# Kernel optimization log

Measured on AMD Instinct MI355X. Metric: run time of the kernel, lower is better.

Reference implementation:

```python
import jax, jax.numpy as jnp
import numpy as np

EMBED_DIM = 1024
N_HEADS = 16
HEAD_DIM = EMBED_DIM // N_HEADS
SCALE = 1.0 / np.sqrt(HEAD_DIM)


def setup_inputs() -> dict:
    key = jax.random.key(0)
    ks = jax.random.split(key, 11)
    B, S, D = 4, 2048, EMBED_DIM
    lim = 1.0 / np.sqrt(D)
    def lin(kk):
        kw, kb = jax.random.split(kk)
        W = jax.random.uniform(kw, (D, D), jnp.float32, -lim, lim)
        b = jax.random.uniform(kb, (D,), jnp.float32, -lim, lim)
        return W, b
    Wq, bq = lin(ks[0])
    Wk, bk = lin(ks[1])
    Wv, bv = lin(ks[2])
    Wo, bo = lin(ks[3])
    q = jax.random.normal(ks[4], (B, S, D), jnp.float32)
    k = jax.random.normal(ks[5], (B, S, D), jnp.float32)
    v = jax.random.normal(ks[6], (B, S, D), jnp.float32)
    return {"q": q, "k": k, "v": v,
            "Wq": Wq, "bq": bq, "Wk": Wk, "bk": bk,
            "Wv": Wv, "bv": bv, "Wo": Wo, "bo": bo}


def reference(q, k, v, Wq, bq, Wk, bk, Wv, bv, Wo, bo):
    B, Sq, D = q.shape
    Sk = k.shape[1]
    # linear projections (torch Linear: x @ W.T + b)
    qh = (q @ Wq.T + bq).reshape(B, Sq, N_HEADS, HEAD_DIM).transpose(0, 2, 1, 3)
    kh = (k @ Wk.T + bk).reshape(B, Sk, N_HEADS, HEAD_DIM).transpose(0, 2, 1, 3)
    vh = (v @ Wv.T + bv).reshape(B, Sk, N_HEADS, HEAD_DIM).transpose(0, 2, 1, 3)
    # scaled dot-product attention, no mask, dropout_p=0
    scores = jnp.einsum('bhqd,bhkd->bhqk', qh, kh) * SCALE  # [B,H,Sq,Sk]
    weights = jax.nn.softmax(scores, axis=-1)
    ctx = jnp.einsum('bhqk,bhkd->bhqd', weights, vh)
    ctx = ctx.transpose(0, 2, 1, 3).reshape(B, Sq, D)
    return ctx @ Wo.T + bo
```

## Files before the change

### kernel.cpp

```cpp
#include <hip/hip_runtime.h>
#include <hip/hip_bf16.h>
#include <stdint.h>

#define B_SZ 4
#define SEQ  2048
#define DM   1024
#define NH   16
#define HD   64
#define MTOT (B_SZ*SEQ)
#define QS_LOG2E 0.18033688011112042f
#define M0SHIFT  24.0f

typedef __attribute__((ext_vector_type(8))) short bf16x8;
typedef __attribute__((ext_vector_type(4))) float f32x4;

#if __has_builtin(__builtin_amdgcn_exp2f)
__device__ __forceinline__ float fexp2(float x) { return __builtin_amdgcn_exp2f(x); }
#else
__device__ __forceinline__ float fexp2(float x) {
  float r; asm("v_exp_f32 %0, %1" : "=v"(r) : "v"(x)); return r;
}
#endif

__device__ __forceinline__ unsigned short f2b(float f) {
  union { float f; unsigned int i; } v; v.f = f;
  unsigned int r = v.i + 0x7fffu + ((v.i >> 16) & 1u);
  return (unsigned short)(r >> 16);
}

#define GPTR __attribute__((address_space(1)))
#define LPTR __attribute__((address_space(3)))
__device__ __forceinline__ void gl_lds16(const void* g, void* l) {
  __builtin_amdgcn_global_load_lds((GPTR const unsigned int*)g,
                                   (LPTR unsigned int*)l, 16, 0, 0);
}

__device__ __forceinline__ void conv_body(const float* __restrict__ in,
                                          unsigned short* __restrict__ out, int n) {
  int i = (blockIdx.x * 256 + threadIdx.x) * 8;
  int stride = gridDim.x * 256 * 8;
  for (; i < n; i += stride) {
    float4 x = *(const float4*)(in + i);
    float4 y = *(const float4*)(in + i + 4);
    ushort4 u0; u0.x = f2b(x.x); u0.y = f2b(x.y); u0.z = f2b(x.z); u0.w = f2b(x.w);
    ushort4 u1; u1.x = f2b(y.x); u1.y = f2b(y.y); u1.z = f2b(y.z); u1.w = f2b(y.w);
    *(ushort4*)(out + i)     = u0;
    *(ushort4*)(out + i + 4) = u1;
  }
}
__global__ __launch_bounds__(256) void conv7(
    const float* __restrict__ q, const float* __restrict__ k, const float* __restrict__ v,
    const float* __restrict__ Wq, const float* __restrict__ Wk,
    const float* __restrict__ Wv, const float* __restrict__ Wo,
    unsigned short* __restrict__ oq, unsigned short* __restrict__ ok,
    unsigned short* __restrict__ ov, unsigned short* __restrict__ oWq,
    unsigned short* __restrict__ oWk, unsigned short* __restrict__ oWv,
    unsigned short* __restrict__ oWo, int nAct, int nW) {
  const int z = blockIdx.z;
  const float* in = (z == 0) ? q : (z == 1) ? k : (z == 2) ? v
                  : (z == 3) ? Wq : (z == 4) ? Wk : (z == 5) ? Wv : Wo;
  unsigned short* out = (z == 0) ? oq : (z == 1) ? ok : (z == 2) ? ov
                      : (z == 3) ? oWq : (z == 4) ? oWk : (z == 5) ? oWv : oWo;
  conv_body(in, out, (z < 3) ? nAct : nW);
}
__global__ __launch_bounds__(256) void conv4(const float* __restrict__ a,
                                             const float* __restrict__ b,
                                             const float* __restrict__ c,
                                             const float* __restrict__ d,
                                             unsigned short* __restrict__ oa,
                                             unsigned short* __restrict__ ob,
                                             unsigned short* __restrict__ oc,
                                             unsigned short* __restrict__ od,
                                             int n) {
  const float* in = (blockIdx.z == 0) ? a : (blockIdx.z == 1) ? b
                  : (blockIdx.z == 2) ? c : d;
  unsigned short* out = (blockIdx.z == 0) ? oa : (blockIdx.z == 1) ? ob
                      : (blockIdx.z == 2) ? oc : od;
  conv_body(in, out, n);
}

__device__ __forceinline__ void stage_glds(const unsigned short* __restrict__ src,
                                           int ld, char* lds, int t) {
  const int gbase = t & ~63;
  const int lane  = t & 63;
  #pragma unroll
  for (int i = 0; i < 4; ++i) {
    int gb  = i*256 + gbase;
    int g   = gb + lane;
    int row = g >> 3;
    int cg  = (g & 7) ^ (row & 7);
    gl_lds16(src + (size_t)row*ld + cg*8, lds + (size_t)gb*16);
  }
}
__device__ __forceinline__ void stage_f32(const float* __restrict__ src, int ld,
                                          unsigned short* lds, int t) {
  #pragma unroll
  for (int i = 0; i < 8; ++i) {
    int e   = i*1024 + t*4;
    int row = e >> 6;
    int c4  = (e >> 2) & 15;
    float4 f = *(const float4*)(src + (size_t)row*ld + c4*4);
    ushort4 u;
    u.x = f2b(f.x); u.y = f2b(f.y); u.z = f2b(f.z); u.w = f2b(f.w);
    int hi = (row*64 + c4*4) ^ ((row & 7) << 3);
    *(ushort4*)&lds[hi] = u;
  }
}

__device__ __forceinline__ void gemm_core_bb(
    const unsigned short* __restrict__ X, const unsigned short* __restrict__ W,
    const float* __restrict__ bias, unsigned short* __restrict__ C,
    float oscale, int m0, int n0, int t,
    unsigned short* As, unsigned short* Bs)
{
  const int lane = t & 63;
  const int w    = t >> 6;
  const int wm   = w >> 1, wn = w & 1;

  f32x4 acc[4][4] = {};

  for (int k0 = 0; k0 < DM; k0 += 64) {
    __syncthreads();
    stage_glds(X + (size_t)m0*DM + k0, DM, (char*)As, t);
    stage_glds(W + (size_t)n0*DM + k0, DM, (char*)Bs, t);
    __syncthreads();

    #pragma unroll
    for (int kk = 0; kk < 2; ++kk) {
      bf16x8 af[4], bfr[4];
      #pragma unroll
      for (int mt = 0; mt < 4; ++mt) {
        int r  = wm*64 + mt*16 + (lane & 15);
        int hi = (r*64 + kk*32 + (lane >> 4)*8) ^ ((r & 7) << 3);
        af[mt] = *(const bf16x8*)&As[hi];
      }
      #pragma unroll
      for (int nt = 0; nt < 4; ++nt) {
        int r  = wn*64 + nt*16 + (lane & 15);
        int hi = (r*64 + kk*32 + (lane >> 4)*8) ^ ((r & 7) << 3);
        bfr[nt] = *(const bf16x8*)&Bs[hi];
      }
      #pragma unroll
      for (int mt = 0; mt < 4; ++mt)
        #pragma unroll
        for (int nt = 0; nt < 4; ++nt)
          acc[mt][nt] = __builtin_amdgcn_mfma_f32_16x16x32_bf16(
              af[mt], bfr[nt], acc[mt][nt], 0, 0, 0);
    }
  }

  #pragma unroll
  for (int nt = 0; nt < 4; ++nt) {
    int col = n0 + wn*64 + nt*16 + (lane & 15);
    float bv = bias[col];
    #pragma unroll
    for (int mt = 0; mt < 4; ++mt) {
      #pragma unroll
      for (int j = 0; j < 4; ++j) {
        int rrow = m0 + wm*64 + mt*16 + (lane >> 4)*4 + j;
        C[(size_t)rrow*DM + col] = f2b((acc[mt][nt][j] + bv) * oscale);
      }
    }
  }
}

__global__ __launch_bounds__(256, 2) void gemm_qkv(
    const unsigned short* __restrict__ Xb, const unsigned short* __restrict__ Wb,
    const float* __restrict__ b0, const float* __restrict__ b1,
    const float* __restrict__ b2, unsigned short* __restrict__ Cb, float os0)
{
  __shared__ __align__(16) unsigned short As[128*64];
  __shared__ __align__(16) unsigned short Bs[128*64];
  const int z = blockIdx.z;
  const size_t MD  = (size_t)MTOT * DM;
  const size_t WSZ = (size_t)DM * DM;
  const unsigned short* X = Xb + (size_t)z * MD;
  const unsigned short* W = Wb + (size_t)z * WSZ;
  const float* bias = (z == 0) ? b0 : (z == 1) ? b1 : b2;
  unsigned short* C = Cb + (size_t)z * MD;
  float oscale = (z == 0) ? os0 : 1.0f;
  gemm_core_bb(X, W, bias, C, oscale,
               blockIdx.y * 128, blockIdx.x * 128, threadIdx.x, As, Bs);
}

template<int AF32, int BF32, int OUTF32>
__global__ __launch_bounds__(256, 2) void gemm_bias(
    const void* __restrict__ Xv,
    const void* __restrict__ Wv,
    const float* __restrict__ bias,
    void* __restrict__ Cout,
    int M, int N, int Kd, float oscale)
{
  __shared__ __align__(16) unsigned short As[128*64];
  __shared__ __align__(16) unsigned short Bs[128*64];
  const int t    = threadIdx.x;
  const int lane = t & 63;
  const int w    = t >> 6;
  const int wm   = w >> 1, wn = w & 1;
  const int m0   = blockIdx.y * 128;
  const int n0   = blockIdx.x * 128;

  f32x4 acc[4][4] = {};

  for (int k0 = 0; k0 < Kd; k0 += 64) {
    __syncthreads();
    if (AF32) stage_f32((const float*)Xv + (size_t)m0*Kd + k0, Kd, As, t);
    else      stage_glds((const unsigned short*)Xv + (size_t)m0*Kd + k0, Kd, (char*)As, t);
    if (BF32) stage_f32((const float*)Wv + (size_t)n0*Kd + k0, Kd, Bs, t);
    else      stage_glds((const unsigned short*)Wv + (size_t)n0*Kd + k0, Kd, (char*)Bs, t);
    __syncthreads();

    #pragma unroll
    for (int kk = 0; kk < 2; ++kk) {
      bf16x8 af[4], bfr[4];
      #pragma unroll
      for (int mt = 0; mt < 4; ++mt) {
        int r  = wm*64 + mt*16 + (lane & 15);
        int hi = (r*64 + kk*32 + (lane >> 4)*8) ^ ((r & 7) << 3);
        af[mt] = *(const bf16x8*)&As[hi];
      }
      #pragma unroll
      for (int nt = 0; nt < 4; ++nt) {
        int r  = wn*64 + nt*16 + (lane & 15);
        int hi = (r*64 + kk*32 + (lane >> 4)*8) ^ ((r & 7) << 3);
        bfr[nt] = *(const bf16x8*)&Bs[hi];
      }
      #pragma unroll
      for (int mt = 0; mt < 4; ++mt)
        #pragma unroll
        for (int nt = 0; nt < 4; ++nt)
          acc[mt][nt] = __builtin_amdgcn_mfma_f32_16x16x32_bf16(
              af[mt], bfr[nt], acc[mt][nt], 0, 0, 0);
    }
  }

  #pragma unroll
  for (int nt = 0; nt < 4; ++nt) {
    int col = n0 + wn*64 + nt*16 + (lane & 15);
    float bv = bias[col];
    #pragma unroll
    for (int mt = 0; mt < 4; ++mt) {
      #pragma unroll
      for (int j = 0; j < 4; ++j) {
        int rrow = m0 + wm*64 + mt*16 + (lane >> 4)*4 + j;
        float val = (acc[mt][nt][j] + bv) * oscale;
        if (OUTF32)
          ((float*)Cout)[(size_t)rrow*N + col] = val;
        else
          ((unsigned short*)Cout)[(size_t)rrow*N + col] = f2b(val);
      }
    }
  }
}

__global__ __launch_bounds__(256, 2) void attn_fwd(
    const unsigned short* __restrict__ Qb,
    const unsigned short* __restrict__ Kb,
    const unsigned short* __restrict__ Vb,
    unsigned short* __restrict__ Ob)
{
  __shared__ __align__(16) unsigned short Buf[4][64*64];

  const int t    = threadIdx.x;
  const int lane = t & 63;
  const int w    = t >> 6;
  const int l15  = lane & 15;
  const int quad = lane >> 4;

  const int id   = blockIdx.x + (int)gridDim.x * blockIdx.y;
  const int r_   = id & 7;
  const int j_   = id >> 3;
  const int bh   = r_*8 + (j_ >> 4);
  const int qt   = j_ & 15;
  const int b    = bh >> 4, h = bh & 15;
  const int q0   = qt * 128;
  const int gbase = t & ~63;

  const size_t headoff = ((size_t)b*SEQ)*DM + (size_t)h*HD;
  const unsigned short* Qh = Qb + headoff;
  const unsigned short* Kh = Kb + headoff;
  const unsigned short* Vh = Vb + headoff;

  const int jp   = (t & 31) * 2;
  const int seg  = t >> 5;
  const int slot0 = ((jp >> 5) & 1)*32 + ((jp >> 2) & 3)*8 + ((jp >> 4) & 1)*4 + (jp & 3);
  const unsigned short* vsrc = Vh + (size_t)jp*DM + seg*8;

  {
    unsigned short* Qlds = &Buf[2][0];
    #pragma unroll
    for (int i = 0; i < 4; ++i) {
      int gb  = i*256 + gbase;
      int g   = gb + lane;
      int row = g >> 3;
      int cg  = (g & 7) ^ (row & 7);
      gl_lds16(Qh + (size_t)(q0 + row)*DM + cg*8, (char*)Qlds + (size_t)gb*16);
    }
  }
  bf16x8 pvA0 = *(const bf16x8*)(vsrc);
  bf16x8 pvA1 = *(const bf16x8*)(vsrc + DM);
  bf16x8 pvB0 = *(const bf16x8*)(vsrc + 64*DM);
  bf16x8 pvB1 = *(const bf16x8*)(vsrc + 65*DM);
  __syncthreads();

  bf16x8 qfA[2], qfB[2];
  {
    const unsigned short* Qlds = &Buf[2][0];
    #pragma unroll
    for (int kk = 0; kk < 2; ++kk) {
      int rA  = w*32 + l15;
      int rB  = w*32 + 16 + l15;
      qfA[kk] = *(const bf16x8*)&Qlds[(rA*64 + kk*32 + quad*8) ^ ((rA & 7) << 3)];
      qfB[kk] = *(const bf16x8*)&Qlds[(rB*64 + kk*32 + quad*8) ^ ((rB & 7) << 3)];
    }
  }
  auto writeV = [&](const bf16x8& v0, const bf16x8& v1, unsigned short* dst) {
    #pragma unroll
    for (int e = 0; e < 8; ++e) {
      int d = seg*8 + e;
      unsigned int pk = (unsigned int)(unsigned short)v0[e]
                      | ((unsigned int)(unsigned short)v1[e] << 16);
      *(unsigned int*)&dst[(d*64 + slot0) ^ ((d & 7) << 3)] = pk;
    }
  };
  writeV(pvA0, pvA1, Buf[0]);
  writeV(pvB0, pvB1, Buf[1]);
  __syncthreads();

  auto stageK = [&](int kv0, unsigned short* dst) {
    #pragma unroll
    for (int i = 0; i < 2; ++i) {
      int gb  = i*256 + gbase;
      int g   = gb + lane;
      int row = g >> 3;
      int cg  = (g & 7) ^ (row & 7);
      gl_lds16(Kh + (size_t)(kv0 + row)*DM + cg*8, (char*)dst + (size_t)gb*16);
    }
  };
  stageK(0,  Buf[2]);
  stageK(64, Buf[3]);
  __syncthreads();

  float lA = 0.f, lB = 0.f;
  f32x4 oA[4] = {}, oB[4] = {};
  const f32x4 mseed = {-M0SHIFT, -M0SHIFT, -M0SHIFT, -M0SHIFT};

  auto tile = [&](const unsigned short* Kc, const unsigned short* Vc) {
    f32x4 sA[4] = {mseed, mseed, mseed, mseed};
    f32x4 sB[4] = {mseed, mseed, mseed, mseed};
    __builtin_amdgcn_s_setprio(1);
    #pragma unroll
    for (int kk = 0; kk < 2; ++kk) {
      #pragma unroll
      for (int nt = 0; nt < 4; ++nt) {
        int r  = nt*16 + l15;
        int hi = (r*64 + kk*32 + quad*8) ^ ((r & 7) << 3);
        bf16x8 kf = *(const bf16x8*)&Kc[hi];
        sA[nt] = __builtin_amdgcn_mfma_f32_16x16x32_bf16(kf, qfA[kk], sA[nt], 0, 0, 0);
        sB[nt] = __builtin_amdgcn_mfma_f32_16x16x32_bf16(kf, qfB[kk], sB[nt], 0, 0, 0);
      }
    }
    __builtin_amdgcn_s_setprio(0);

    union { bf16x8 v; unsigned int u[4]; } PA0, PA1, PB0, PB1;
    {
      float p[4][4]; float rs = 0.f;
      #pragma unroll
      for (int nt = 0; nt < 4; ++nt)
        #pragma unroll
        for (int j = 0; j < 4; ++j) { p[nt][j] = fexp2(sA[nt][j]); rs += p[nt][j]; }
      lA += rs;
      #pragma unroll
      for (int k2 = 0; k2 < 4; ++k2) {
        int nt = k2 >> 1, a = (k2 & 1)*2;
        asm("v_cvt_pk_bf16_f32 %0, %1, %2" : "=v"(PA0.u[k2]) : "v"(p[nt][a]), "v"(p[nt][a+1]));
        asm("v_cvt_pk_bf16_f32 %0, %1, %2" : "=v"(PA1.u[k2]) : "v"(p[2+nt][a]), "v"(p[2+nt][a+1]));
      }
    }
    {
      float p[4][4]; float rs = 0.f;
      #pragma unroll
      for (int nt = 0; nt < 4; ++nt)
        #pragma unroll
        for (int j = 0; j < 4; ++j) { p[nt][j] = fexp2(sB[nt][j]); rs += p[nt][j]; }
      lB += rs;
      #pragma unroll
      for (int k2 = 0; k2 < 4; ++k2) {
        int nt = k2 >> 1, a = (k2 & 1)*2;
        asm("v_cvt_pk_bf16_f32 %0, %1, %2" : "=v"(PB0.u[k2]) : "v"(p[nt][a]), "v"(p[nt][a+1]));
        asm("v_cvt_pk_bf16_f32 %0, %1, %2" : "=v"(PB1.u[k2]) : "v"(p[2+nt][a]), "v"(p[2+nt][a+1]));
      }
    }

    __builtin_amdgcn_s_setprio(1);
    #pragma unroll
    for (int ks = 0; ks < 2; ++ks) {
      bf16x8 pfA = ks ? PA1.v : PA0.v;
      bf16x8 pfB = ks ? PB1.v : PB0.v;
      #pragma unroll
      for (int dt = 0; dt < 4; ++dt) {
        int d  = dt*16 + l15;
        int hi = (d*64 + ks*32 + quad*8) ^ ((d & 7) << 3);
        bf16x8 vf = *(const bf16x8*)&Vc[hi];
        oA[dt] = __builtin_amdgcn_mfma_f32_16x16x32_bf16(vf, pfA, oA[dt], 0, 0, 0);
        oB[dt] = __builtin_amdgcn_mfma_f32_16x16x32_bf16(vf, pfB, oB[dt], 0, 0, 0);
      }
    }
    __builtin_amdgcn_s_setprio(0);
  };

  for (int tk = 0; tk < SEQ/64; tk += 2) {
    const bool pa = (tk + 2 < SEQ/64);
    const bool pb = (tk + 3 < SEQ/64);
    if (pa) {
      const unsigned short* s = vsrc + (size_t)(tk + 2)*64*DM;
      pvA0 = *(const bf16x8*)(s);
      pvA1 = *(const bf16x8*)(s + DM);
    }
    tile(Buf[2], Buf[0]);
    __syncthreads();
    if (pa) { stageK((tk + 2)*64, Buf[2]); writeV(pvA0, pvA1, Buf[0]); }
    if (pb) {
      const unsigned short* s = vsrc + (size_t)(tk + 3)*64*DM;
      pvB0 = *(const bf16x8*)(s);
      pvB1 = *(const bf16x8*)(s + DM);
    }
    tile(Buf[3], Buf[1]);
    __syncthreads();
    if (pb) { stageK((tk + 3)*64, Buf[3]); writeV(pvB0, pvB1, Buf[1]); }
  }

  {
    float la = lA, lb = lB;
    la += __shfl_xor(la, 16); la += __shfl_xor(la, 32);
    lb += __shfl_xor(lb, 16); lb += __shfl_xor(lb, 32);
    float rla = 1.0f / la, rlb = 1.0f / lb;
    int qrowA = q0 + w*32 + l15;
    int qrowB = qrowA + 16;
    #pragma unroll
    for (int dt = 0; dt < 4; ++dt) {
      ushort4 u;
      u.x = f2b(oA[dt][0]*rla); u.y = f2b(oA[dt][1]*rla);
      u.z = f2b(oA[dt][2]*rla); u.w = f2b(oA[dt][3]*rla);
      *(ushort4*)&Ob[headoff + (size_t)qrowA*DM + dt*16 + quad*4] = u;
      ushort4 v;
      v.x = f2b(oB[dt][0]*rlb); v.y = f2b(oB[dt][1]*rlb);
      v.z = f2b(oB[dt][2]*rlb); v.w = f2b(oB[dt][3]*rlb);
      *(ushort4*)&Ob[headoff + (size_t)qrowB*DM + dt*16 + quad*4] = v;
    }
  }
}

extern "C" void kernel_launch(void* const* d_in, const int* in_sizes, int n_in,
                              void* d_out, int out_size, void* d_ws, size_t ws_size,
                              hipStream_t stream) {
  const float* q  = (const float*)d_in[0];
  const float* k  = (const float*)d_in[1];
  const float* v  = (const float*)d_in[2];
  const float* Wq = (const float*)d_in[3];
  const float* bq = (const float*)d_in[4];
  const float* Wk = (const float*)d_in[5];
  const float* bk = (const float*)d_in[6];
  const float* Wv = (const float*)d_in[7];
  const float* bv = (const float*)d_in[8];
  const float* Wo = (const float*)d_in[9];
  const float* bo = (const float*)d_in[10];

  const size_t MD  = (size_t)MTOT * DM;
  const size_t WSZ = (size_t)DM * DM;
  unsigned short* ws = (unsigned short*)d_ws;

  dim3 blk(256);
  dim3 gproj(DM/128, MTOT/128);
  dim3 gattn(SEQ/128, B_SZ*NH);

  const size_t need_big = (6*MD + 4*WSZ) * 2;
  const size_t need_mid = (4*MD + 1*WSZ) * 2;

  if (ws_size >= need_big) {
    unsigned short* qB  = ws;
    unsigned short* kB  = ws + MD;
    unsigned short* vB  = ws + 2*MD;
    unsigned short* Qp  = ws + 3*MD;
    unsigned short* Kp  = ws + 4*MD;
    unsigned short* Vp  = ws + 5*MD;
    unsigned short* WqB = ws + 6*MD;
    unsigned short* WoB = WqB + 3*WSZ;
    unsigned short* Cp  = qB;

    hipLaunchKernelGGL(conv7, dim3(1024,1,7), blk, 0, stream,
                       q, k, v, Wq, Wk, Wv, Wo,
                       qB, kB, vB, WqB, WqB + WSZ, WqB + 2*WSZ, WoB,
                       (int)MD, (int)WSZ);

    hipLaunchKernelGGL(gemm_qkv, dim3(DM/128, MTOT/128, 3), blk, 0, stream,
                       qB, WqB, bq, bk, bv, Qp, QS_LOG2E);

    hipLaunchKernelGGL(attn_fwd, gattn, blk, 0, stream, Qp, Kp, Vp, Cp);
    hipLaunchKernelGGL((gemm_bias<0,0,1>), gproj, blk, 0, stream, (const void*)Cp, (const void*)WoB, bo, d_out, MTOT, DM, DM, 1.0f);
  } else if (ws_size >= need_mid) {
    unsigned short* Qp  = ws;
    unsigned short* Kp  = ws + MD;
    unsigned short* Vp  = ws + 2*MD;
    unsigned short* Cp  = ws + 3*MD;
    unsigned short* WqB = Cp;
    unsigned short* WkB = Cp + WSZ;
    unsigned short* WvB = Cp + 2*WSZ;
    unsigned short* WoB = ws + 4*MD;

    hipLaunchKernelGGL(conv4, dim3(512,1,4), blk, 0, stream, Wq, Wk, Wv, Wo, WqB, WkB, WvB, WoB, (int)WSZ);

    hipLaunchKernelGGL((gemm_bias<1,0,0>), gproj, blk, 0, stream, (const void*)q, (const void*)WqB, bq, (void*)Qp, MTOT, DM, DM, QS_LOG2E);
    hipLaunchKernelGGL((gemm_bias<1,0,0>), gproj, blk, 0, stream, (const void*)k, (const void*)WkB, bk, (void*)Kp, MTOT, DM, DM, 1.0f);
    hipLaunchKernelGGL((gemm_bias<1,0,0>), gproj, blk, 0, stream, (const void*)v, (const void*)WvB, bv, (void*)Vp, MTOT, DM, DM, 1.0f);
    hipLaunchKernelGGL(attn_fwd, gattn, blk, 0, stream, Qp, Kp, Vp, Cp);
    hipLaunchKernelGGL((gemm_bias<0,0,1>), gproj, blk, 0, stream, (const void*)Cp, (const void*)WoB, bo, d_out, MTOT, DM, DM, 1.0f);
  } else {
    unsigned short* Qp = ws;
    unsigned short* Kp = ws + MD;
    unsigned short* Vp = ws + 2*MD;
    unsigned short* Cp = ws + 3*MD;

    hipLaunchKernelGGL((gemm_bias<1,1,0>), gproj, blk, 0, stream, (const void*)q, (const void*)Wq, bq, (void*)Qp, MTOT, DM, DM, QS_LOG2E);
    hipLaunchKernelGGL((gemm_bias<1,1,0>), gproj, blk, 0, stream, (const void*)k, (const void*)Wk, bk, (void*)Kp, MTOT, DM, DM, 1.0f);
    hipLaunchKernelGGL((gemm_bias<1,1,0>), gproj, blk, 0, stream, (const void*)v, (const void*)Wv, bv, (void*)Vp, MTOT, DM, DM, 1.0f);
    hipLaunchKernelGGL(attn_fwd, gattn, blk, 0, stream, Qp, Kp, Vp, Cp);
    hipLaunchKernelGGL((gemm_bias<0,1,1>), gproj, blk, 0, stream, (const void*)Cp, (const void*)Wo, bo, d_out, MTOT, DM, DM, 1.0f);
  }
}
```

Baseline: 216.8 us.

## Swizzle GEMM block order for L2 reuse and add bf16 output-projection kernel

Remaps block indices in the QKV GEMM into grouped tiles of eight M-rows by eight N-columns, so concurrently running blocks share A and B tiles in L2. Adds a gemm_o128 kernel with the same grouped ordering that uses the global-to-LDS bf16 core with fp32 output, replacing the generic gemm_bias for the output projection. It also packs V pairs with a byte-permute instruction instead of shifts and ors. The remapping assumes fixed grid dimensions (8 by 64 by 3 and 8 by 64).

```diff
diff --git a/kernel.cpp b/kernel.cpp
--- a/kernel.cpp
+++ b/kernel.cpp
@@ -107,9 +107,10 @@
   }
 }
 
+template<int OUTF32>
 __device__ __forceinline__ void gemm_core_bb(
     const unsigned short* __restrict__ X, const unsigned short* __restrict__ W,
-    const float* __restrict__ bias, unsigned short* __restrict__ C,
+    const float* __restrict__ bias, void* __restrict__ C,
     float oscale, int m0, int n0, int t,
     unsigned short* As, unsigned short* Bs)
 {
@@ -158,7 +159,9 @@
       #pragma unroll
       for (int j = 0; j < 4; ++j) {
         int rrow = m0 + wm*64 + mt*16 + (lane >> 4)*4 + j;
-        C[(size_t)rrow*DM + col] = f2b((acc[mt][nt][j] + bv) * oscale);
+        float val = (acc[mt][nt][j] + bv) * oscale;
+        if (OUTF32) ((float*)C)[(size_t)rrow*DM + col] = val;
+        else        ((unsigned short*)C)[(size_t)rrow*DM + col] = f2b(val);
       }
     }
   }
@@ -171,16 +174,32 @@
 {
   __shared__ __align__(16) unsigned short As[128*64];
   __shared__ __align__(16) unsigned short Bs[128*64];
-  const int z = blockIdx.z;
+  const int id = blockIdx.x + 8*blockIdx.y + 512*blockIdx.z;
+  const int r_ = id & 7;
+  const int xn = (id >> 3) & 7;
+  const int G  = (id >> 6)*8 + r_;
+  const int y  = G & 63;
+  const int z  = G >> 6;
   const size_t MD  = (size_t)MTOT * DM;
   const size_t WSZ = (size_t)DM * DM;
-  const unsigned short* X = Xb + (size_t)z * MD;
-  const unsigned short* W = Wb + (size_t)z * WSZ;
   const float* bias = (z == 0) ? b0 : (z == 1) ? b1 : b2;
-  unsigned short* C = Cb + (size_t)z * MD;
-  float oscale = (z == 0) ? os0 : 1.0f;
-  gemm_core_bb(X, W, bias, C, oscale,
-               blockIdx.y * 128, blockIdx.x * 128, threadIdx.x, As, Bs);
+  gemm_core_bb<0>(Xb + (size_t)z*MD, Wb + (size_t)z*WSZ, bias,
+                  (void*)(Cb + (size_t)z*MD), (z == 0) ? os0 : 1.0f,
+                  y * 128, xn * 128, threadIdx.x, As, Bs);
+}
+
+__global__ __launch_bounds__(256, 2) void gemm_o128(
+    const unsigned short* __restrict__ X, const unsigned short* __restrict__ W,
+    const float* __restrict__ bias, float* __restrict__ C)
+{
+  __shared__ __align__(16) unsigned short As[128*64];
+  __shared__ __align__(16) unsigned short Bs[128*64];
+  const int id = blockIdx.x + 8*blockIdx.y;
+  const int r_ = id & 7;
+  const int xn = (id >> 3) & 7;
+  const int y  = (id >> 6)*8 + r_;
+  gemm_core_bb<1>(X, W, bias, (void*)C, 1.0f,
+                  y * 128, xn * 128, threadIdx.x, As, Bs);
 }
 
 template<int AF32, int BF32, int OUTF32>
@@ -315,11 +334,14 @@
     }
   }
   auto writeV = [&](const bf16x8& v0, const bf16x8& v1, unsigned short* dst) {
+    const unsigned int* v0w = (const unsigned int*)&v0;
+    const unsigned int* v1w = (const unsigned int*)&v1;
     #pragma unroll
     for (int e = 0; e < 8; ++e) {
       int d = seg*8 + e;
-      unsigned int pk = (unsigned int)(unsigned short)v0[e]
-                      | ((unsigned int)(unsigned short)v1[e] << 16);
+      unsigned int pk = __builtin_amdgcn_perm(
+          v1w[e >> 1], v0w[e >> 1],
+          (e & 1) ? 0x07060302u : 0x05040100u);
       *(unsigned int*)&dst[(d*64 + slot0) ^ ((d & 7) << 3)] = pk;
     }
   };
@@ -497,7 +519,8 @@
                        qB, WqB, bq, bk, bv, Qp, QS_LOG2E);
 
     hipLaunchKernelGGL(attn_fwd, gattn, blk, 0, stream, Qp, Kp, Vp, Cp);
-    hipLaunchKernelGGL((gemm_bias<0,0,1>), gproj, blk, 0, stream, (const void*)Cp, (const void*)WoB, bo, d_out, MTOT, DM, DM, 1.0f);
+
+    hipLaunchKernelGGL(gemm_o128, gproj, blk, 0, stream, Cp, WoB, bo, (float*)d_out);
   } else if (ws_size >= need_mid) {
     unsigned short* Qp  = ws;
     unsigned short* Kp  = ws + MD;
```

New measurement: 206.5 us, median of 2. 4.8% less time.
